# Kernel tuning notes

Hardware: AMD Instinct MI355X
Metric: run time of the kernel (lower is better)

## Reference

```python
import jax, jax.numpy as jnp
import numpy as np

B, S, D = 4, 1024, 1024
DH = D // 8  # q/k projection dim


def setup_inputs() -> dict:
    key = jax.random.key(0)
    ks = jax.random.split(key, 16)
    std = 0.02
    inp = {
        "drums": jax.random.normal(ks[0], (B, S, D), jnp.float32),
        "vocals": jax.random.normal(ks[1], (B, S, D), jnp.float32),
        "bass": jax.random.normal(ks[2], (B, S, D), jnp.float32),
        "other": jax.random.normal(ks[3], (B, S, D), jnp.float32),
        # Linear weights stored [in, out] (transposed vs torch's [out, in])
        "DqW": jax.random.normal(ks[4], (D, DH), jnp.float32) * std,
        "Dqb": jax.random.normal(ks[5], (DH,), jnp.float32) * std,
        "DkW": jax.random.normal(ks[6], (D, DH), jnp.float32) * std,
        "Dkb": jax.random.normal(ks[7], (DH,), jnp.float32) * std,
        "DvW": jax.random.normal(ks[8], (D, D), jnp.float32) * std,
        "Dvb": jax.random.normal(ks[9], (D,), jnp.float32) * std,
        "VqW": jax.random.normal(ks[10], (D, DH), jnp.float32) * std,
        "Vqb": jax.random.normal(ks[11], (DH,), jnp.float32) * std,
        "VkW": jax.random.normal(ks[12], (D, DH), jnp.float32) * std,
        "Vkb": jax.random.normal(ks[13], (DH,), jnp.float32) * std,
        "VvW": jax.random.normal(ks[14], (D, D), jnp.float32) * std,
        "Vvb": jax.random.normal(ks[15], (D,), jnp.float32) * std,
    }
    return inp


def reference(drums, vocals, bass, other,
              DqW, Dqb, DkW, Dkb, DvW, Dvb,
              VqW, Vqb, VkW, Vkb, VvW, Vvb):
    d_model = drums.shape[-1]
    lin = lambda x, W, b: jnp.einsum("bsd,de->bse", x, W) + b
    # drums uses D_* projections; vocals/bass/other all use V_* (faithful to source)
    q = jnp.concatenate([lin(drums, DqW, Dqb), lin(vocals, VqW, Vqb),
                         lin(bass, VqW, Vqb), lin(other, VqW, Vqb)], axis=-2)
    k = jnp.concatenate([lin(drums, DkW, Dkb), lin(vocals, VkW, Vkb),
                         lin(bass, VkW, Vkb), lin(other, VkW, Vkb)], axis=-2)
    v = jnp.concatenate([lin(drums, DvW, Dvb), lin(vocals, VvW, Vvb),
                         lin(bass, VvW, Vvb), lin(other, VvW, Vvb)], axis=-2)
    # scores: [B, 4S, 4S]; dropout is identity at inference
    scores = jnp.einsum("bqe,bke->bqk", q, k) / jnp.sqrt(jnp.asarray(d_model, q.dtype))
    attn = jax.nn.softmax(scores, axis=-1)
    out = jnp.einsum("bqk,bkd->bqd", attn, v)  # [B, 4S, D]
    return out.mean(axis=-2)  # [B, D]
```

## Files before the change

### kernel.cpp

```cpp
#include <hip/hip_runtime.h>
#include <hip/hip_bf16.h>

typedef __bf16 bf16x8 __attribute__((ext_vector_type(8)));
typedef float  f32x4  __attribute__((ext_vector_type(4)));

#define MFMA_16x16x32(a, b, c) __builtin_amdgcn_mfma_f32_16x16x32_bf16((a), (b), (c), 0, 0, 0)

static constexpr float SCALE  = 0.03125f;
static constexpr float INV_NQ = 1.0f / 4096.0f;

__device__ inline bf16x8 ld_cvt_bf8(const float* __restrict__ p) {
    f32x4 x0 = *(const f32x4*)p;
    f32x4 x1 = *(const f32x4*)(p + 4);
    bf16x8 r;
    r[0] = (__bf16)x0[0]; r[1] = (__bf16)x0[1]; r[2] = (__bf16)x0[2]; r[3] = (__bf16)x0[3];
    r[4] = (__bf16)x1[0]; r[5] = (__bf16)x1[1]; r[6] = (__bf16)x1[2]; r[7] = (__bf16)x1[3];
    return r;
}

__global__ __launch_bounds__(256) void kT(const float* __restrict__ Dq, const float* __restrict__ Vq,
                                          const float* __restrict__ Dk, const float* __restrict__ Vk,
                                          __bf16* __restrict__ Wt) {
    int idx = blockIdx.x * 256 + threadIdx.x;
    int m   = idx >> 17;
    int rem = idx & 131071;
    int r   = rem >> 7;
    int c   = rem & 127;
    const float* W = (m == 0) ? Dq : (m == 1) ? Vq : (m == 2) ? Dk : Vk;
    Wt[(size_t)m * 131072 + (size_t)c * 1024 + r] = (__bf16)W[rem];
}

__global__ __launch_bounds__(256) void kProj(
    const float* __restrict__ drums, const float* __restrict__ vocals,
    const float* __restrict__ bass,  const float* __restrict__ other,
    const float* __restrict__ Dqb, const float* __restrict__ Vqb,
    const float* __restrict__ Dkb, const float* __restrict__ Vkb,
    const __bf16* __restrict__ Wt, __bf16* __restrict__ Qb, __bf16* __restrict__ Kb) {
    int bx   = blockIdx.x;
    int qk   = bx >> 7;
    int tile = bx & 127;
    int grow0 = tile * 128;
    int b    = grow0 >> 12;
    int r4   = grow0 & 4095;
    int stem = r4 >> 10;
    int rin  = r4 & 1023;

    const float* X = (stem == 0) ? drums : (stem == 1) ? vocals : (stem == 2) ? bass : other;
    const __bf16* W;
    const float* bias;
    if (qk == 0) { W = Wt + (size_t)((stem == 0) ? 0 : 1) * 131072; bias = (stem == 0) ? Dqb : Vqb; }
    else         { W = Wt + (size_t)((stem == 0) ? 2 : 3) * 131072; bias = (stem == 0) ? Dkb : Vkb; }
    __bf16* Out = (qk == 0) ? Qb : Kb;

    int lane = threadIdx.x & 63, wid = threadIdx.x >> 6;
    int l16 = lane & 15, g = lane >> 4;
    int wr = rin + wid * 32;

    f32x4 acc[2][8];
#pragma unroll
    for (int i = 0; i < 2; i++)
#pragma unroll
        for (int j = 0; j < 8; j++) acc[i][j] = (f32x4){0.f, 0.f, 0.f, 0.f};

    const float* xr0 = X + ((size_t)b * 1024 + wr + l16) * 1024;
    const float* xr1 = xr0 + 16 * 1024;
    for (int k0 = 0; k0 < 1024; k0 += 32) {
        int ko = k0 + g * 8;
        bf16x8 a0 = ld_cvt_bf8(xr0 + ko);
        bf16x8 a1 = ld_cvt_bf8(xr1 + ko);
#pragma unroll
        for (int cf = 0; cf < 8; cf++) {
            bf16x8 bv = *(const bf16x8*)(W + (size_t)(cf * 16 + l16) * 1024 + ko);
            acc[0][cf] = MFMA_16x16x32(a0, bv, acc[0][cf]);
            acc[1][cf] = MFMA_16x16x32(a1, bv, acc[1][cf]);
        }
    }
    size_t obase = (size_t)b * 4096 + (size_t)stem * 1024;
#pragma unroll
    for (int rf = 0; rf < 2; rf++)
#pragma unroll
        for (int cf = 0; cf < 8; cf++) {
            int col = cf * 16 + l16;
            float bv = bias[col];
#pragma unroll
            for (int r = 0; r < 4; r++) {
                int row = wr + rf * 16 + g * 4 + r;
                Out[(obase + row) * 128 + col] = (__bf16)(acc[rf][cf][r] + bv);
            }
        }
}

__global__ __launch_bounds__(256) void kRowSum(const __bf16* __restrict__ Qb,
                                               const __bf16* __restrict__ Kb,
                                               float* __restrict__ lsum) {
    int bx = blockIdx.x;
    int half = bx & 1;
    int rest = bx >> 1;
    int b = rest >> 5, tile = rest & 31;
    int lane = threadIdx.x & 63, wid = threadIdx.x >> 6;
    int l16 = lane & 15, g = lane >> 4;
    int R = tile * 128 + wid * 32;
    const __bf16* Qr = Qb + (size_t)b * 4096 * 128;
    const __bf16* Kr = Kb + (size_t)b * 4096 * 128;

    bf16x8 a[2][4];
#pragma unroll
    for (int rf = 0; rf < 2; rf++)
#pragma unroll
        for (int kf = 0; kf < 4; kf++)
            a[rf][kf] = *(const bf16x8*)(Qr + (size_t)(R + rf * 16 + l16) * 128 + kf * 32 + g * 8);

    float rs[2][4] = {};
    for (int ct = half * 128; ct < half * 128 + 128; ct++) {
        f32x4 acc0 = (f32x4){0.f, 0.f, 0.f, 0.f};
        f32x4 acc1 = (f32x4){0.f, 0.f, 0.f, 0.f};
#pragma unroll
        for (int kf = 0; kf < 4; kf++) {
            bf16x8 bv = *(const bf16x8*)(Kr + (size_t)(ct * 16 + l16) * 128 + kf * 32 + g * 8);
            acc0 = MFMA_16x16x32(a[0][kf], bv, acc0);
            acc1 = MFMA_16x16x32(a[1][kf], bv, acc1);
        }
#pragma unroll
        for (int r = 0; r < 4; r++) {
            rs[0][r] += __expf(acc0[r] * SCALE);
            rs[1][r] += __expf(acc1[r] * SCALE);
        }
    }
#pragma unroll
    for (int rf = 0; rf < 2; rf++)
#pragma unroll
        for (int r = 0; r < 4; r++) {
            float v = rs[rf][r];
#pragma unroll
            for (int m = 1; m < 16; m <<= 1) v += __shfl_xor(v, m);
            if (l16 == 0) atomicAdd(&lsum[(size_t)b * 4096 + R + rf * 16 + g * 4 + r], v);
        }
}

__global__ __launch_bounds__(256) void kColSum(const __bf16* __restrict__ Qb,
                                               const __bf16* __restrict__ Kb,
                                               const float* __restrict__ lsum,
                                               float* __restrict__ wsum) {
    __shared__ float linv[4096];
    int bx = blockIdx.x;
    int half = bx & 1;
    int rest = bx >> 1;
    int b = rest >> 5, tile = rest & 31;
    const float* lb = lsum + (size_t)b * 4096;
    for (int i = threadIdx.x; i < 4096; i += 256) linv[i] = 1.0f / lb[i];
    __syncthreads();

    int lane = threadIdx.x & 63, wid = threadIdx.x >> 6;
    int l16 = lane & 15, g = lane >> 4;
    int C = tile * 128 + wid * 32;
    const __bf16* Qr = Qb + (size_t)b * 4096 * 128;
    const __bf16* Kr = Kb + (size_t)b * 4096 * 128;

    bf16x8 kb[2][4];
#pragma unroll
    for (int cf = 0; cf < 2; cf++)
#pragma unroll
        for (int kf = 0; kf < 4; kf++)
            kb[cf][kf] = *(const bf16x8*)(Kr + (size_t)(C + cf * 16 + l16) * 128 + kf * 32 + g * 8);

    float cs[2] = {0.f, 0.f};
    for (int rt = half * 128; rt < half * 128 + 128; rt++) {
        f32x4 acc0 = (f32x4){0.f, 0.f, 0.f, 0.f};
        f32x4 acc1 = (f32x4){0.f, 0.f, 0.f, 0.f};
#pragma unroll
        for (int kf = 0; kf < 4; kf++) {
            bf16x8 av = *(const bf16x8*)(Qr + (size_t)(rt * 16 + l16) * 128 + kf * 32 + g * 8);
            acc0 = MFMA_16x16x32(av, kb[0][kf], acc0);
            acc1 = MFMA_16x16x32(av, kb[1][kf], acc1);
        }
#pragma unroll
        for (int r = 0; r < 4; r++) {
            float li = linv[rt * 16 + g * 4 + r];
            cs[0] += __expf(acc0[r] * SCALE) * li;
            cs[1] += __expf(acc1[r] * SCALE) * li;
        }
    }
#pragma unroll
    for (int cf = 0; cf < 2; cf++) {
        float v = cs[cf];
        v += __shfl_xor(v, 16);
        v += __shfl_xor(v, 32);
        if (lane < 16) atomicAdd(&wsum[(size_t)b * 4096 + C + cf * 16 + lane], v);
    }
}

__global__ __launch_bounds__(256) void kY(
    const float* __restrict__ drums, const float* __restrict__ vocals,
    const float* __restrict__ bass,  const float* __restrict__ other,
    const float* __restrict__ wsum, float* __restrict__ y, float* __restrict__ alpha) {
    __shared__ float ws[128];
    int bx = blockIdx.x;
    int b = bx >> 5, stem = (bx >> 3) & 3, kc = bx & 7;
    const float* X = (stem == 0) ? drums : (stem == 1) ? vocals : (stem == 2) ? bass : other;
    int t = threadIdx.x;
    if (t < 128) ws[t] = wsum[(size_t)b * 4096 + stem * 1024 + kc * 128 + t] * INV_NQ;
    __syncthreads();

    f32x4 acc = (f32x4){0.f, 0.f, 0.f, 0.f};
    const float* xp = X + ((size_t)b * 1024 + kc * 128) * 1024 + t * 4;
    for (int i = 0; i < 128; i++) {
        f32x4 xv = *(const f32x4*)(xp + (size_t)i * 1024);
        float wv = ws[i];
        acc[0] += wv * xv[0]; acc[1] += wv * xv[1]; acc[2] += wv * xv[2]; acc[3] += wv * xv[3];
    }
    int seg = (stem == 0) ? 0 : 1;
    float* yp = y + ((size_t)b * 2 + seg) * 1024 + t * 4;
    atomicAdd(yp + 0, acc[0]); atomicAdd(yp + 1, acc[1]);
    atomicAdd(yp + 2, acc[2]); atomicAdd(yp + 3, acc[3]);

    if (t < 64) {
        float s = ws[t] + ws[t + 64];
#pragma unroll
        for (int m = 32; m > 0; m >>= 1) s += __shfl_down(s, m);
        if (t == 0) atomicAdd(alpha + b * 2 + seg, s);
    }
}

__global__ __launch_bounds__(256) void kFinal(
    const float* __restrict__ DvW, const float* __restrict__ Dvb,
    const float* __restrict__ VvW, const float* __restrict__ Vvb,
    const float* __restrict__ y, const float* __restrict__ alpha,
    float* __restrict__ out) {
    __shared__ float yD[256], yV[256];
    int bx = blockIdx.x;
    int b = bx >> 4, dstripe = (bx >> 2) & 3, kc = bx & 3;
    int t = threadIdx.x;
    yD[t] = y[((size_t)b * 2 + 0) * 1024 + kc * 256 + t];
    yV[t] = y[((size_t)b * 2 + 1) * 1024 + kc * 256 + t];
    __syncthreads();

    int d = dstripe * 256 + t;
    const float* pD = DvW + (size_t)(kc * 256) * 1024 + d;
    const float* pV = VvW + (size_t)(kc * 256) * 1024 + d;
    float acc = 0.f;
#pragma unroll 4
    for (int k = 0; k < 256; k++)
        acc += yD[k] * pD[(size_t)k * 1024] + yV[k] * pV[(size_t)k * 1024];
    if (kc == 0) acc += alpha[b * 2] * Dvb[d] + alpha[b * 2 + 1] * Vvb[d];
    atomicAdd(out + (size_t)b * 1024 + d, acc);
}

extern "C" void kernel_launch(void* const* d_in, const int* in_sizes, int n_in,
                              void* d_out, int out_size, void* d_ws, size_t ws_size,
                              hipStream_t stream) {
    const float* drums  = (const float*)d_in[0];
    const float* vocals = (const float*)d_in[1];
    const float* bass   = (const float*)d_in[2];
    const float* other  = (const float*)d_in[3];
    const float* DqW = (const float*)d_in[4];
    const float* Dqb = (const float*)d_in[5];
    const float* DkW = (const float*)d_in[6];
    const float* Dkb = (const float*)d_in[7];
    const float* DvW = (const float*)d_in[8];
    const float* Dvb = (const float*)d_in[9];
    const float* VqW = (const float*)d_in[10];
    const float* Vqb = (const float*)d_in[11];
    const float* VkW = (const float*)d_in[12];
    const float* Vkb = (const float*)d_in[13];
    const float* VvW = (const float*)d_in[14];
    const float* Vvb = (const float*)d_in[15];
    float* out = (float*)d_out;

    char* ws = (char*)d_ws;
    __bf16* Qb   = (__bf16*)(ws);
    __bf16* Kb   = (__bf16*)(ws + (4u << 20));
    __bf16* Wt   = (__bf16*)(ws + (8u << 20));
    float*  lsum = (float*)(ws + (9u << 20));
    float*  wsum = (float*)(ws + (9u << 20) + (64u << 10));
    float*  y    = (float*)(ws + (9u << 20) + (128u << 10));
    float*  alph = (float*)(ws + (9u << 20) + (160u << 10));

    hipMemsetAsync(lsum, 0, (160u << 10) + 32, stream);
    hipMemsetAsync(out, 0, (size_t)out_size * sizeof(float), stream);

    kT<<<2048, 256, 0, stream>>>(DqW, VqW, DkW, VkW, Wt);
    kProj<<<256, 256, 0, stream>>>(drums, vocals, bass, other, Dqb, Vqb, Dkb, Vkb, Wt, Qb, Kb);
    kRowSum<<<256, 256, 0, stream>>>(Qb, Kb, lsum);
    kColSum<<<256, 256, 0, stream>>>(Qb, Kb, lsum, wsum);
    kY<<<128, 256, 0, stream>>>(drums, vocals, bass, other, wsum, y, alph);
    kFinal<<<64, 256, 0, stream>>>(DvW, Dvb, VvW, Vvb, y, alph, out);
}
```

Before: 383.3 us.

## Stage K/Q tiles in swizzled LDS, fuse Q/K projection, widen grids

```diff
diff --git a/kernel.cpp b/kernel.cpp
--- a/kernel.cpp
+++ b/kernel.cpp
@@ -4,9 +4,9 @@
 typedef __bf16 bf16x8 __attribute__((ext_vector_type(8)));
 typedef float  f32x4  __attribute__((ext_vector_type(4)));
 
-#define MFMA_16x16x32(a, b, c) __builtin_amdgcn_mfma_f32_16x16x32_bf16((a), (b), (c), 0, 0, 0)
-
-static constexpr float SCALE  = 0.03125f;
+#define MFMA(a, b, c) __builtin_amdgcn_mfma_f32_16x16x32_bf16((a), (b), (c), 0, 0, 0)
+
+static constexpr float SC_L2E = 0.03125f * 1.44269504088896341f;
 static constexpr float INV_NQ = 1.0f / 4096.0f;
 
 __device__ inline bf16x8 ld_cvt_bf8(const float* __restrict__ p) {
@@ -36,70 +36,62 @@
     const float* __restrict__ Dqb, const float* __restrict__ Vqb,
     const float* __restrict__ Dkb, const float* __restrict__ Vkb,
     const __bf16* __restrict__ Wt, __bf16* __restrict__ Qb, __bf16* __restrict__ Kb) {
-    int bx   = blockIdx.x;
-    int qk   = bx >> 7;
-    int tile = bx & 127;
-    int grow0 = tile * 128;
+    int grow0 = blockIdx.x * 64;
     int b    = grow0 >> 12;
     int r4   = grow0 & 4095;
     int stem = r4 >> 10;
     int rin  = r4 & 1023;
 
     const float* X = (stem == 0) ? drums : (stem == 1) ? vocals : (stem == 2) ? bass : other;
-    const __bf16* W;
-    const float* bias;
-    if (qk == 0) { W = Wt + (size_t)((stem == 0) ? 0 : 1) * 131072; bias = (stem == 0) ? Dqb : Vqb; }
-    else         { W = Wt + (size_t)((stem == 0) ? 2 : 3) * 131072; bias = (stem == 0) ? Dkb : Vkb; }
-    __bf16* Out = (qk == 0) ? Qb : Kb;
+    const __bf16* WQ = Wt + (size_t)((stem == 0) ? 0 : 1) * 131072;
+    const __bf16* WK = Wt + (size_t)((stem == 0) ? 2 : 3) * 131072;
+    const float* bQ = (stem == 0) ? Dqb : Vqb;
+    const float* bK = (stem == 0) ? Dkb : Vkb;
 
     int lane = threadIdx.x & 63, wid = threadIdx.x >> 6;
     int l16 = lane & 15, g = lane >> 4;
-    int wr = rin + wid * 32;
-
-    f32x4 acc[2][8];
-#pragma unroll
-    for (int i = 0; i < 2; i++)
-#pragma unroll
-        for (int j = 0; j < 8; j++) acc[i][j] = (f32x4){0.f, 0.f, 0.f, 0.f};
-
-    const float* xr0 = X + ((size_t)b * 1024 + wr + l16) * 1024;
-    const float* xr1 = xr0 + 16 * 1024;
+    int wr = rin + wid * 16;
+
+    f32x4 aQ[8], aK[8];
+#pragma unroll
+    for (int j = 0; j < 8; j++) { aQ[j] = (f32x4){0.f,0.f,0.f,0.f}; aK[j] = (f32x4){0.f,0.f,0.f,0.f}; }
+
+    const float* xr = X + ((size_t)b * 1024 + wr + l16) * 1024;
     for (int k0 = 0; k0 < 1024; k0 += 32) {
         int ko = k0 + g * 8;
-        bf16x8 a0 = ld_cvt_bf8(xr0 + ko);
-        bf16x8 a1 = ld_cvt_bf8(xr1 + ko);
+        bf16x8 a = ld_cvt_bf8(xr + ko);
 #pragma unroll
         for (int cf = 0; cf < 8; cf++) {
-            bf16x8 bv = *(const bf16x8*)(W + (size_t)(cf * 16 + l16) * 1024 + ko);
-            acc[0][cf] = MFMA_16x16x32(a0, bv, acc[0][cf]);
-            acc[1][cf] = MFMA_16x16x32(a1, bv, acc[1][cf]);
+            bf16x8 wq = *(const bf16x8*)(WQ + (size_t)(cf * 16 + l16) * 1024 + ko);
+            aQ[cf] = MFMA(a, wq, aQ[cf]);
+            bf16x8 wk = *(const bf16x8*)(WK + (size_t)(cf * 16 + l16) * 1024 + ko);
+            aK[cf] = MFMA(a, wk, aK[cf]);
         }
     }
     size_t obase = (size_t)b * 4096 + (size_t)stem * 1024;
 #pragma unroll
-    for (int rf = 0; rf < 2; rf++)
-#pragma unroll
-        for (int cf = 0; cf < 8; cf++) {
-            int col = cf * 16 + l16;
-            float bv = bias[col];
-#pragma unroll
-            for (int r = 0; r < 4; r++) {
-                int row = wr + rf * 16 + g * 4 + r;
-                Out[(obase + row) * 128 + col] = (__bf16)(acc[rf][cf][r] + bv);
-            }
-        }
+    for (int cf = 0; cf < 8; cf++) {
+        int col = cf * 16 + l16;
+        float bvq = bQ[col], bvk = bK[col];
+#pragma unroll
+        for (int r = 0; r < 4; r++) {
+            int row = wr + g * 4 + r;
+            Qb[(obase + row) * 128 + col] = (__bf16)(aQ[cf][r] + bvq);
+            Kb[(obase + row) * 128 + col] = (__bf16)(aK[cf][r] + bvk);
+        }
+    }
 }
 
 __global__ __launch_bounds__(256) void kRowSum(const __bf16* __restrict__ Qb,
                                                const __bf16* __restrict__ Kb,
                                                float* __restrict__ lsum) {
+    __shared__ uint4 ktile[1024];
     int bx = blockIdx.x;
-    int half = bx & 1;
-    int rest = bx >> 1;
-    int b = rest >> 5, tile = rest & 31;
+    int cc = bx & 7, tile = (bx >> 3) & 31, b = bx >> 8;
     int lane = threadIdx.x & 63, wid = threadIdx.x >> 6;
     int l16 = lane & 15, g = lane >> 4;
-    int R = tile * 128 + wid * 32;
+    int R  = tile * 128 + wid * 32;
+    int C0 = cc * 512;
     const __bf16* Qr = Qb + (size_t)b * 4096 * 128;
     const __bf16* Kr = Kb + (size_t)b * 4096 * 128;
 
@@ -110,20 +102,46 @@
         for (int kf = 0; kf < 4; kf++)
             a[rf][kf] = *(const bf16x8*)(Qr + (size_t)(R + rf * 16 + l16) * 128 + kf * 32 + g * 8);
 
+    int sr = threadIdx.x >> 2, sseg = threadIdx.x & 3;
+    char* kbc = (char*)ktile;
+    int swm = (sr & 7) << 4;
+
+    uint4 st[4];
+    {
+        const char* src = (const char*)(Kr + (size_t)(C0 + sr) * 128) + sseg * 64;
+#pragma unroll
+        for (int j = 0; j < 4; j++) st[j] = *(const uint4*)(src + j * 16);
+    }
+
     float rs[2][4] = {};
-    for (int ct = half * 128; ct < half * 128 + 128; ct++) {
-        f32x4 acc0 = (f32x4){0.f, 0.f, 0.f, 0.f};
-        f32x4 acc1 = (f32x4){0.f, 0.f, 0.f, 0.f};
-#pragma unroll
-        for (int kf = 0; kf < 4; kf++) {
-            bf16x8 bv = *(const bf16x8*)(Kr + (size_t)(ct * 16 + l16) * 128 + kf * 32 + g * 8);
-            acc0 = MFMA_16x16x32(a[0][kf], bv, acc0);
-            acc1 = MFMA_16x16x32(a[1][kf], bv, acc1);
-        }
-#pragma unroll
-        for (int r = 0; r < 4; r++) {
-            rs[0][r] += __expf(acc0[r] * SCALE);
-            rs[1][r] += __expf(acc1[r] * SCALE);
+    for (int s = 0; s < 8; ++s) {
+        __syncthreads();
+#pragma unroll
+        for (int j = 0; j < 4; j++)
+            *(uint4*)(kbc + sr * 256 + ((sseg * 64 + j * 16) ^ swm)) = st[j];
+        __syncthreads();
+        if (s < 7) {
+            const char* src = (const char*)(Kr + (size_t)(C0 + (s + 1) * 64 + sr) * 128) + sseg * 64;
+#pragma unroll
+            for (int j = 0; j < 4; j++) st[j] = *(const uint4*)(src + j * 16);
+        }
+#pragma unroll
+        for (int ctl = 0; ctl < 4; ++ctl) {
+            int r2 = ctl * 16 + l16;
+            int rm = (r2 & 7) << 4;
+            f32x4 acc0 = (f32x4){0.f,0.f,0.f,0.f};
+            f32x4 acc1 = (f32x4){0.f,0.f,0.f,0.f};
+#pragma unroll
+            for (int kf = 0; kf < 4; kf++) {
+                bf16x8 bv = *(const bf16x8*)(kbc + r2 * 256 + ((kf * 64 + g * 16) ^ rm));
+                acc0 = MFMA(a[0][kf], bv, acc0);
+                acc1 = MFMA(a[1][kf], bv, acc1);
+            }
+#pragma unroll
+            for (int r = 0; r < 4; r++) {
+                rs[0][r] += exp2f(acc0[r] * SC_L2E);
+                rs[1][r] += exp2f(acc1[r] * SC_L2E);
+            }
         }
     }
 #pragma unroll
@@ -137,25 +155,31 @@
         }
 }
 
+__global__ __launch_bounds__(256) void kInv(const float* __restrict__ lsum, float* __restrict__ linv) {
+    int i = (blockIdx.x * 256 + threadIdx.x) * 4;
+    f32x4 v = *(const f32x4*)(lsum + i);
+    f32x4 r = (f32x4){1.f / v[0], 1.f / v[1], 1.f / v[2], 1.f / v[3]};
+    *(f32x4*)(linv + i) = r;
+}
+
 __global__ __launch_bounds__(256) void kColSum(const __bf16* __restrict__ Qb,
                                                const __bf16* __restrict__ Kb,
-                                               const float* __restrict__ lsum,
+                                               const float* __restrict__ linv,
                                                float* __restrict__ wsum) {
-    __shared__ float linv[4096];
+    __shared__ uint4 qtile[1024];
+    __shared__ float li[512];
     int bx = blockIdx.x;
-    int half = bx & 1;
-    int rest = bx >> 1;
-    int b = rest >> 5, tile = rest & 31;
-    const float* lb = lsum + (size_t)b * 4096;
-    for (int i = threadIdx.x; i < 4096; i += 256) linv[i] = 1.0f / lb[i];
-    __syncthreads();
-
+    int rc = bx & 7, tile = (bx >> 3) & 31, b = bx >> 8;
     int lane = threadIdx.x & 63, wid = threadIdx.x >> 6;
     int l16 = lane & 15, g = lane >> 4;
-    int C = tile * 128 + wid * 32;
+    int C  = tile * 128 + wid * 32;
+    int R0 = rc * 512;
     const __bf16* Qr = Qb + (size_t)b * 4096 * 128;
     const __bf16* Kr = Kb + (size_t)b * 4096 * 128;
 
+    if (threadIdx.x < 128)
+        *(f32x4*)(li + threadIdx.x * 4) = *(const f32x4*)(linv + (size_t)b * 4096 + R0 + threadIdx.x * 4);
+
     bf16x8 kb[2][4];
 #pragma unroll
     for (int cf = 0; cf < 2; cf++)
@@ -163,21 +187,48 @@
         for (int kf = 0; kf < 4; kf++)
             kb[cf][kf] = *(const bf16x8*)(Kr + (size_t)(C + cf * 16 + l16) * 128 + kf * 32 + g * 8);
 
+    int sr = threadIdx.x >> 2, sseg = threadIdx.x & 3;
+    char* qbc = (char*)qtile;
+    int swm = (sr & 7) << 4;
+
+    uint4 st[4];
+    {
+        const char* src = (const char*)(Qr + (size_t)(R0 + sr) * 128) + sseg * 64;
+#pragma unroll
+        for (int j = 0; j < 4; j++) st[j] = *(const uint4*)(src + j * 16);
+    }
+
     float cs[2] = {0.f, 0.f};
-    for (int rt = half * 128; rt < half * 128 + 128; rt++) {
-        f32x4 acc0 = (f32x4){0.f, 0.f, 0.f, 0.f};
-        f32x4 acc1 = (f32x4){0.f, 0.f, 0.f, 0.f};
-#pragma unroll
-        for (int kf = 0; kf < 4; kf++) {
-            bf16x8 av = *(const bf16x8*)(Qr + (size_t)(rt * 16 + l16) * 128 + kf * 32 + g * 8);
-            acc0 = MFMA_16x16x32(av, kb[0][kf], acc0);
-            acc1 = MFMA_16x16x32(av, kb[1][kf], acc1);
-        }
-#pragma unroll
-        for (int r = 0; r < 4; r++) {
-            float li = linv[rt * 16 + g * 4 + r];
-            cs[0] += __expf(acc0[r] * SCALE) * li;
-            cs[1] += __expf(acc1[r] * SCALE) * li;
+    for (int s = 0; s < 8; ++s) {
+        __syncthreads();
+#pragma unroll
+        for (int j = 0; j < 4; j++)
+            *(uint4*)(qbc + sr * 256 + ((sseg * 64 + j * 16) ^ swm)) = st[j];
+        __syncthreads();
+        if (s < 7) {
+            const char* src = (const char*)(Qr + (size_t)(R0 + (s + 1) * 64 + sr) * 128) + sseg * 64;
+#pragma unroll
+            for (int j = 0; j < 4; j++) st[j] = *(const uint4*)(src + j * 16);
+        }
+#pragma unroll
+        for (int ctl = 0; ctl < 4; ++ctl) {
+            int r2 = ctl * 16 + l16;
+            int rm = (r2 & 7) << 4;
+            f32x4 acc0 = (f32x4){0.f,0.f,0.f,0.f};
+            f32x4 acc1 = (f32x4){0.f,0.f,0.f,0.f};
+#pragma unroll
+            for (int kf = 0; kf < 4; kf++) {
+                bf16x8 av = *(const bf16x8*)(qbc + r2 * 256 + ((kf * 64 + g * 16) ^ rm));
+                acc0 = MFMA(av, kb[0][kf], acc0);
+                acc1 = MFMA(av, kb[1][kf], acc1);
+            }
+            int ib = s * 64 + ctl * 16 + g * 4;
+#pragma unroll
+            for (int r = 0; r < 4; r++) {
+                float lv = li[ib + r];
+                cs[0] += exp2f(acc0[r] * SC_L2E) * lv;
+                cs[1] += exp2f(acc1[r] * SC_L2E) * lv;
+            }
         }
     }
 #pragma unroll
@@ -193,17 +244,18 @@
     const float* __restrict__ drums, const float* __restrict__ vocals,
     const float* __restrict__ bass,  const float* __restrict__ other,
     const float* __restrict__ wsum, float* __restrict__ y, float* __restrict__ alpha) {
-    __shared__ float ws[128];
+    __shared__ float ws[64];
     int bx = blockIdx.x;
-    int b = bx >> 5, stem = (bx >> 3) & 3, kc = bx & 7;
+    int b = bx >> 6, stem = (bx >> 4) & 3, kc = bx & 15;
     const float* X = (stem == 0) ? drums : (stem == 1) ? vocals : (stem == 2) ? bass : other;
     int t = threadIdx.x;
-    if (t < 128) ws[t] = wsum[(size_t)b * 4096 + stem * 1024 + kc * 128 + t] * INV_NQ;
+    if (t < 64) ws[t] = wsum[(size_t)b * 4096 + stem * 1024 + kc * 64 + t] * INV_NQ;
     __syncthreads();
 
     f32x4 acc = (f32x4){0.f, 0.f, 0.f, 0.f};
-    const float* xp = X + ((size_t)b * 1024 + kc * 128) * 1024 + t * 4;
-    for (int i = 0; i < 128; i++) {
+    const float* xp = X + ((size_t)b * 1024 + kc * 64) * 1024 + t * 4;
+#pragma unroll 4
+    for (int i = 0; i < 64; i++) {
         f32x4 xv = *(const f32x4*)(xp + (size_t)i * 1024);
         float wv = ws[i];
         acc[0] += wv * xv[0]; acc[1] += wv * xv[1]; acc[2] += wv * xv[2]; acc[3] += wv * xv[3];
@@ -214,7 +266,7 @@
     atomicAdd(yp + 2, acc[2]); atomicAdd(yp + 3, acc[3]);
 
     if (t < 64) {
-        float s = ws[t] + ws[t + 64];
+        float s = ws[t];
 #pragma unroll
         for (int m = 32; m > 0; m >>= 1) s += __shfl_down(s, m);
         if (t == 0) atomicAdd(alpha + b * 2 + seg, s);
@@ -226,20 +278,22 @@
     const float* __restrict__ VvW, const float* __restrict__ Vvb,
     const float* __restrict__ y, const float* __restrict__ alpha,
     float* __restrict__ out) {
-    __shared__ float yD[256], yV[256];
+    __shared__ float yD[128], yV[128];
     int bx = blockIdx.x;
-    int b = bx >> 4, dstripe = (bx >> 2) & 3, kc = bx & 3;
+    int b = bx >> 5, dstripe = (bx >> 3) & 3, kc = bx & 7;
     int t = threadIdx.x;
-    yD[t] = y[((size_t)b * 2 + 0) * 1024 + kc * 256 + t];
-    yV[t] = y[((size_t)b * 2 + 1) * 1024 + kc * 256 + t];
+    if (t < 128) {
+        yD[t] = y[((size_t)b * 2 + 0) * 1024 + kc * 128 + t];
+        yV[t] = y[((size_t)b * 2 + 1) * 1024 + kc * 128 + t];
+    }
     __syncthreads();
 
     int d = dstripe * 256 + t;
-    const float* pD = DvW + (size_t)(kc * 256) * 1024 + d;
-    const float* pV = VvW + (size_t)(kc * 256) * 1024 + d;
+    const float* pD = DvW + (size_t)(kc * 128) * 1024 + d;
+    const float* pV = VvW + (size_t)(kc * 128) * 1024 + d;
     float acc = 0.f;
 #pragma unroll 4
-    for (int k = 0; k < 256; k++)
+    for (int k = 0; k < 128; k++)
         acc += yD[k] * pD[(size_t)k * 1024] + yV[k] * pV[(size_t)k * 1024];
     if (kc == 0) acc += alpha[b * 2] * Dvb[d] + alpha[b * 2 + 1] * Vvb[d];
     atomicAdd(out + (size_t)b * 1024 + d, acc);
@@ -274,14 +328,16 @@
     float*  wsum = (float*)(ws + (9u << 20) + (64u << 10));
     float*  y    = (float*)(ws + (9u << 20) + (128u << 10));
     float*  alph = (float*)(ws + (9u << 20) + (160u << 10));
+    float*  linv = (float*)(ws + (9u << 20) + (192u << 10));
 
     hipMemsetAsync(lsum, 0, (160u << 10) + 32, stream);
     hipMemsetAsync(out, 0, (size_t)out_size * sizeof(float), stream);
 
     kT<<<2048, 256, 0, stream>>>(DqW, VqW, DkW, VkW, Wt);
     kProj<<<256, 256, 0, stream>>>(drums, vocals, bass, other, Dqb, Vqb, Dkb, Vkb, Wt, Qb, Kb);
-    kRowSum<<<256, 256, 0, stream>>>(Qb, Kb, lsum);
-    kColSum<<<256, 256, 0, stream>>>(Qb, Kb, lsum, wsum);
-    kY<<<128, 256, 0, stream>>>(drums, vocals, bass, other, wsum, y, alph);
-    kFinal<<<64, 256, 0, stream>>>(DvW, Dvb, VvW, Vvb, y, alph, out);
-}
+    kRowSum<<<1024, 256, 0, stream>>>(Qb, Kb, lsum);
+    kInv<<<16, 256, 0, stream>>>(lsum, linv);
+    kColSum<<<1024, 256, 0, stream>>>(Qb, Kb, linv, wsum);
+    kY<<<256, 256, 0, stream>>>(drums, vocals, bass, other, wsum, y, alph);
+    kFinal<<<128, 256, 0, stream>>>(DvW, Dvb, VvW, Vvb, y, alph, out);
+}
```

Measured after the change: 329.7 us. 14.0% less time.
